# Optimization experiments

Measured on AMD Instinct MI355X. Metric: run time of the kernel, lower is better.

The kernel has to match this reference:

```python
import jax, jax.numpy as jnp
import numpy as np

N = 100000   # nodes
E = 1600000  # edges
F = 128      # in_feats
H = 4        # heads
D = 32       # out_feats per head
NEG_SLOPE = 0.2


def setup_inputs() -> dict:
    key = jax.random.key(0)
    k1, k2, k3, k4, k5, k6 = jax.random.split(key, 6)
    feat = jax.random.normal(k1, (N, F), dtype=jnp.float32)
    W = jax.random.normal(k2, (H * D, F), dtype=jnp.float32) * (1.0 / np.sqrt(F))
    attn_l = jax.random.normal(k3, (1, H, D), dtype=jnp.float32) * 0.1
    attn_r = jax.random.normal(k4, (1, H, D), dtype=jnp.float32) * 0.1
    src = jax.random.randint(k5, (E,), 0, N, dtype=jnp.int32)
    dst = jax.random.randint(k6, (E,), 0, N, dtype=jnp.int32)
    return {"feat": feat, "W": W, "attn_l": attn_l, "attn_r": attn_r, "src": src, "dst": dst}


def reference(feat, W, attn_l, attn_r, src, dst):
    # fc projection: [N, F] -> [N, H, D]
    h = (feat @ W.T).reshape(N, H, D)
    # per-node attention logits [N, H]
    el = jnp.sum(h * attn_l, axis=-1)
    er = jnp.sum(h * attn_r, axis=-1)
    # edge scores: el[src] + er[dst] -> leaky relu  [E, H]
    e = jax.nn.leaky_relu(el[src] + er[dst], negative_slope=NEG_SLOPE)
    # segment softmax over edges grouped by destination node, per head
    m = jax.ops.segment_max(e, dst, num_segments=N)          # [N, H]
    ex = jnp.exp(e - m[dst])                                 # [E, H]
    s = jax.ops.segment_sum(ex, dst, num_segments=N)         # [N, H]
    alpha = ex / s[dst]                                      # [E, H]
    # weighted sparse aggregation: out[dst] += alpha * h[src]
    msgs = alpha[:, :, None] * h[src]                        # [E, H, D]
    rst = jax.ops.segment_sum(msgs, dst, num_segments=N)     # [N, H, D]
    return rst
```

## Files before the change

### kernel.cpp

```cpp
#include <hip/hip_runtime.h>

constexpr int N_NODES = 100000;
constexpr int E_EDGES = 1600000;
constexpr int NBLK    = (N_NODES + 1023) / 1024;

typedef _Float16 f16;
typedef _Float16 f16x2 __attribute__((ext_vector_type(2)));
typedef _Float16 f16x4 __attribute__((ext_vector_type(4)));
typedef _Float16 f16x8 __attribute__((ext_vector_type(8)));
typedef float f32x4 __attribute__((ext_vector_type(4)));

__global__ __launch_bounds__(256) void k_gemm(const float* __restrict__ feat,
                                              const float* __restrict__ W,
                                              const float* __restrict__ attn_l,
                                              const float* __restrict__ attn_r,
                                              f16* __restrict__ h2,
                                              float* __restrict__ el,
                                              float* __restrict__ er) {
    __shared__ f16 Wlds[128 * 128];
    char* wb = (char*)Wlds;
    const int tid = threadIdx.x;

    {
        int n = tid >> 1;
        int kh = (tid & 1) * 64;
        const float* wsrc = W + n * 128 + kh;
#pragma unroll
        for (int q = 0; q < 8; ++q) {
            float4 u0 = *reinterpret_cast<const float4*>(wsrc + q * 8);
            float4 u1 = *reinterpret_cast<const float4*>(wsrc + q * 8 + 4);
            f16x8 v;
            v[0] = (f16)u0.x; v[1] = (f16)u0.y; v[2] = (f16)u0.z; v[3] = (f16)u0.w;
            v[4] = (f16)u1.x; v[5] = (f16)u1.y; v[6] = (f16)u1.z; v[7] = (f16)u1.w;
            unsigned byte = (unsigned)(n * 256 + kh * 2 + q * 16) ^ ((n & 7) << 4);
            *reinterpret_cast<f16x8*>(wb + byte) = v;
        }
    }
    __syncthreads();

    const int wav  = tid >> 6;
    const int lane = tid & 63;
    const int la = lane & 15;
    const int lb = lane >> 4;
    const int row0w = blockIdx.x * 64 + wav * 16;

    f16x8 ffrag[4];
    {
        int rowA = row0w + la;
        if (rowA >= N_NODES) rowA = N_NODES - 1;
        const float* ap = feat + (size_t)rowA * 128 + lb * 8;
#pragma unroll
        for (int kk = 0; kk < 4; ++kk) {
            float4 u0 = *reinterpret_cast<const float4*>(ap + kk * 32);
            float4 u1 = *reinterpret_cast<const float4*>(ap + kk * 32 + 4);
            f16x8 a;
            a[0] = (f16)u0.x; a[1] = (f16)u0.y; a[2] = (f16)u0.z; a[3] = (f16)u0.w;
            a[4] = (f16)u1.x; a[5] = (f16)u1.y; a[6] = (f16)u1.z; a[7] = (f16)u1.w;
            ffrag[kk] = a;
        }
    }

    f32x4 acc[8];
#pragma unroll
    for (int t = 0; t < 8; ++t) acc[t] = (f32x4){0.f, 0.f, 0.f, 0.f};

#pragma unroll
    for (int t = 0; t < 8; ++t) {
        int wrow = t * 16 + la;
#pragma unroll
        for (int kk = 0; kk < 4; ++kk) {
            unsigned byte = (unsigned)(wrow * 256 + (kk * 32 + lb * 8) * 2) ^ ((wrow & 7) << 4);
            f16x8 b = *reinterpret_cast<const f16x8*>(wb + byte);
            acc[t] = __builtin_amdgcn_mfma_f32_16x16x32_f16(b, ffrag[kk], acc[t], 0, 0, 0);
        }
    }

    const int row = row0w + la;
    const bool ok = row < N_NODES;
    if (ok) {
#pragma unroll
        for (int t = 0; t < 8; ++t) {
            f16x4 hv;
            hv.x = (f16)acc[t][0]; hv.y = (f16)acc[t][1];
            hv.z = (f16)acc[t][2]; hv.w = (f16)acc[t][3];
            *reinterpret_cast<f16x4*>(&h2[(size_t)row * 128 + t * 16 + lb * 4]) = hv;
        }
    }

    float sl[4] = {0.f, 0.f, 0.f, 0.f}, sr[4] = {0.f, 0.f, 0.f, 0.f};
#pragma unroll
    for (int t = 0; t < 8; ++t) {
        float4 alv = reinterpret_cast<const float4*>(attn_l)[t * 4 + lb];
        float4 arv = reinterpret_cast<const float4*>(attn_r)[t * 4 + lb];
        int g = t >> 1;
        sl[g] += acc[t][0] * alv.x + acc[t][1] * alv.y + acc[t][2] * alv.z + acc[t][3] * alv.w;
        sr[g] += acc[t][0] * arv.x + acc[t][1] * arv.y + acc[t][2] * arv.z + acc[t][3] * arv.w;
    }
#pragma unroll
    for (int g = 0; g < 4; ++g) {
        sl[g] += __shfl_xor(sl[g], 16, 64);
        sl[g] += __shfl_xor(sl[g], 32, 64);
        sr[g] += __shfl_xor(sr[g], 16, 64);
        sr[g] += __shfl_xor(sr[g], 32, 64);
    }
    if (lb == 0 && ok) {
        *reinterpret_cast<float4*>(el + (size_t)row * 4) = make_float4(sl[0], sl[1], sl[2], sl[3]);
        *reinterpret_cast<float4*>(er + (size_t)row * 4) = make_float4(sr[0], sr[1], sr[2], sr[3]);
    }
}

__global__ void k_hist(const int4* __restrict__ dst4, int* __restrict__ deg,
                       int4* __restrict__ rank4) {
    int t = blockIdx.x * blockDim.x + threadIdx.x;
    if (t < E_EDGES / 4) {
        int4 d = dst4[t];
        int r0 = atomicAdd(&deg[d.x], 1);
        int r1 = atomicAdd(&deg[d.y], 1);
        int r2 = atomicAdd(&deg[d.z], 1);
        int r3 = atomicAdd(&deg[d.w], 1);
        rank4[t] = make_int4(r0, r1, r2, r3);
    }
}

__global__ void k_bsum(const int* __restrict__ deg, int* __restrict__ aux) {
    int tid = threadIdx.x;
    int i0 = blockIdx.x * 1024 + tid * 4;
    int sum = 0;
#pragma unroll
    for (int j = 0; j < 4; ++j)
        if (i0 + j < N_NODES) sum += (deg[i0 + j] + 3) & ~3;
#pragma unroll
    for (int m = 32; m; m >>= 1) sum += __shfl_xor(sum, m, 64);
    __shared__ int wsums[4];
    if ((tid & 63) == 0) wsums[tid >> 6] = sum;
    __syncthreads();
    if (tid == 0) aux[blockIdx.x] = wsums[0] + wsums[1] + wsums[2] + wsums[3];
}

__global__ void k_scanaux(int* __restrict__ aux) {
    __shared__ int s[128];
    int i = threadIdx.x;
    int v = (i < NBLK) ? aux[i] : 0;
    s[i] = v;
    __syncthreads();
#pragma unroll
    for (int d = 1; d < 128; d <<= 1) {
        int t = (i >= d) ? s[i - d] : 0;
        __syncthreads();
        s[i] += t;
        __syncthreads();
    }
    if (i < NBLK) aux[i] = s[i] - v;
}

__global__ void k_bscan(const int* __restrict__ deg, const int* __restrict__ aux,
                        int* __restrict__ start, int* __restrict__ ssrc,
                        f16* __restrict__ h2, float* __restrict__ el) {
    if (blockIdx.x == 0 && threadIdx.x == 0) {
        float4 z = make_float4(0.f, 0.f, 0.f, 0.f);
        float4* hrow = reinterpret_cast<float4*>(h2 + (size_t)N_NODES * 128);
#pragma unroll
        for (int q = 0; q < 16; ++q) hrow[q] = z;
        *reinterpret_cast<float4*>(el + (size_t)N_NODES * 4) =
            make_float4(-1e4f, -1e4f, -1e4f, -1e4f);
    }
    int tid = threadIdx.x;
    int lane = tid & 63;
    int wid = tid >> 6;
    int i0 = blockIdx.x * 1024 + tid * 4;
    int v[4], pv[4];
#pragma unroll
    for (int j = 0; j < 4; ++j) {
        v[j]  = (i0 + j < N_NODES) ? deg[i0 + j] : 0;
        pv[j] = (v[j] + 3) & ~3;
    }
    int tsum = pv[0] + pv[1] + pv[2] + pv[3];
    int x = tsum;
#pragma unroll
    for (int d = 1; d < 64; d <<= 1) {
        int t = __shfl_up(x, d, 64);
        if (lane >= d) x += t;
    }
    __shared__ int wsums[4];
    if (lane == 63) wsums[wid] = x;
    __syncthreads();
    int base = aux[blockIdx.x];
#pragma unroll
    for (int w = 0; w < 4; ++w)
        if (w < wid) base += wsums[w];
    int p = base + x - tsum;
#pragma unroll
    for (int j = 0; j < 4; ++j) {
        if (i0 + j < N_NODES) {
            start[i0 + j] = p;
            for (int q = v[j]; q < pv[j]; ++q) ssrc[p + q] = N_NODES;
        }
        p += pv[j];
    }
}

__global__ void k_scatter(const int* __restrict__ src, const int* __restrict__ dst,
                          const int* __restrict__ rank, const int* __restrict__ start,
                          int* __restrict__ ssrc) {
    int e = blockIdx.x * blockDim.x + threadIdx.x;
    if (e < E_EDGES) ssrc[start[dst[e]] + rank[e]] = src[e];
}

__global__ __launch_bounds__(128) void k_aggr(const f16* __restrict__ h2,
                                              const float* __restrict__ el,
                                              const float* __restrict__ er,
                                              const int* __restrict__ ssrc,
                                              const int* __restrict__ start,
                                              const int* __restrict__ deg,
                                              float* __restrict__ out) {
    int n = blockIdx.x * 2 + (threadIdx.x >> 6);
    if (n >= N_NODES) return;
    int lane = threadIdx.x & 63;
    int g = lane >> 4;
    int d = deg[n];
    int pd = (d + 3) & ~3;
    int s0 = __builtin_amdgcn_readfirstlane(start[n]);
    float ern = er[n * 4 + g];

    f16x2 ac0 = {0, 0}, ac1 = {0, 0}, ac2 = {0, 0}, ac3 = {0, 0};
    f16x2 sw0 = {0, 0}, sw1 = {0, 0}, sw2 = {0, 0}, sw3 = {0, 0};

    for (int i = 0; i < pd; i += 4) {
        int n0 = ssrc[s0 + i];
        int n1 = ssrc[s0 + i + 1];
        int n2 = ssrc[s0 + i + 2];
        int n3 = ssrc[s0 + i + 3];
        float e0 = el[(size_t)n0 * 4 + g];
        float e1 = el[(size_t)n1 * 4 + g];
        float e2 = el[(size_t)n2 * 4 + g];
        float e3 = el[(size_t)n3 * 4 + g];
        f16x2 q0 = reinterpret_cast<const f16x2*>(h2 + (size_t)n0 * 128)[lane];
        f16x2 q1 = reinterpret_cast<const f16x2*>(h2 + (size_t)n1 * 128)[lane];
        f16x2 q2 = reinterpret_cast<const f16x2*>(h2 + (size_t)n2 * 128)[lane];
        f16x2 q3 = reinterpret_cast<const f16x2*>(h2 + (size_t)n3 * 128)[lane];

        float x0 = e0 + ern; x0 = fmaxf(x0, 0.2f * x0);
        float x1 = e1 + ern; x1 = fmaxf(x1, 0.2f * x1);
        float x2 = e2 + ern; x2 = fmaxf(x2, 0.2f * x2);
        float x3 = e3 + ern; x3 = fmaxf(x3, 0.2f * x3);
        float w0 = __expf(x0);
        float w1 = __expf(x1);
        float w2 = __expf(x2);
        float w3 = __expf(x3);

        f16 a0 = (f16)w0; f16x2 wv0 = {a0, a0};
        f16 a1 = (f16)w1; f16x2 wv1 = {a1, a1};
        f16 a2 = (f16)w2; f16x2 wv2 = {a2, a2};
        f16 a3 = (f16)w3; f16x2 wv3 = {a3, a3};

        ac0 += wv0 * q0; sw0 += wv0;
        ac1 += wv1 * q1; sw1 += wv1;
        ac2 += wv2 * q2; sw2 += wv2;
        ac3 += wv3 * q3; sw3 += wv3;
    }

    f16x2 ac = (ac0 + ac1) + (ac2 + ac3);
    f16x2 sw = (sw0 + sw1) + (sw2 + sw3);
    float swf = (float)sw[0];
    float inv = (d > 0) ? 1.0f / swf : 0.0f;
    float2 o = make_float2((float)ac[0] * inv, (float)ac[1] * inv);
    reinterpret_cast<float2*>(out + (size_t)n * 128)[lane] = o;
}

extern "C" void kernel_launch(void* const* d_in, const int* in_sizes, int n_in,
                              void* d_out, int out_size, void* d_ws, size_t ws_size,
                              hipStream_t stream) {
    const float* feat   = (const float*)d_in[0];
    const float* W      = (const float*)d_in[1];
    const float* attn_l = (const float*)d_in[2];
    const float* attn_r = (const float*)d_in[3];
    const int*   src    = (const int*)d_in[4];
    const int*   dst    = (const int*)d_in[5];
    float* out = (float*)d_out;

    f16*   h2    = (f16*)d_ws;
    float* el    = (float*)(h2 + (size_t)(N_NODES + 8) * 128);
    float* er    = el + (size_t)(N_NODES + 4) * 4;
    int*   deg   = (int*)(er + (size_t)N_NODES * 4);
    int*   start = deg + N_NODES;
    int*   rank  = start + N_NODES;
    int*   ssrc  = rank + E_EDGES;
    int*   aux   = ssrc + E_EDGES + 3 * N_NODES + 64;

    hipMemsetAsync(deg, 0, N_NODES * sizeof(int), stream);

    k_hist<<<(E_EDGES / 4 + 255) / 256, 256, 0, stream>>>((const int4*)dst, deg, (int4*)rank);
    k_gemm<<<(N_NODES + 63) / 64, 256, 0, stream>>>(feat, W, attn_l, attn_r, h2, el, er);
    k_bsum<<<NBLK, 256, 0, stream>>>(deg, aux);
    k_scanaux<<<1, 128, 0, stream>>>(aux);
    k_bscan<<<NBLK, 256, 0, stream>>>(deg, aux, start, ssrc, h2, el);
    k_scatter<<<(E_EDGES + 255) / 256, 256, 0, stream>>>(src, dst, rank, start, ssrc);
    k_aggr<<<(N_NODES + 1) / 2, 128, 0, stream>>>(h2, el, er, ssrc, start, deg, out);
}
```

Measured before the change: 211.7 us.

## Merge scan into single-block kernel and split aggregation wave into edge halves

Replaces the three-kernel degree scan (block sums, aux scan, block scan) with one 1024-thread single-block kernel where each thread scans 98 nodes serially, removing two launches and their dependencies. The aggregation kernel now has each half-wave process a different edge with 4 halfs per lane, then combines the halves with cross-lane shuffles. The softmax denominator is accumulated in fp32. The single-block scan has strided, uncoalesced per-thread reads and runs on one CU, and the aggregation adds shuffle-reduction overhead.

```diff
diff --git a/kernel.cpp b/kernel.cpp
--- a/kernel.cpp
+++ b/kernel.cpp
@@ -2,7 +2,6 @@
 
 constexpr int N_NODES = 100000;
 constexpr int E_EDGES = 1600000;
-constexpr int NBLK    = (N_NODES + 1023) / 1024;
 
 typedef _Float16 f16;
 typedef _Float16 f16x2 __attribute__((ext_vector_type(2)));
@@ -122,80 +121,48 @@
     }
 }
 
-__global__ void k_bsum(const int* __restrict__ deg, int* __restrict__ aux) {
-    int tid = threadIdx.x;
-    int i0 = blockIdx.x * 1024 + tid * 4;
+__global__ __launch_bounds__(1024) void k_scan(const int* __restrict__ deg,
+                                               int* __restrict__ start,
+                                               int* __restrict__ ssrc,
+                                               f16* __restrict__ h2,
+                                               float* __restrict__ el) {
+    const int t = threadIdx.x;
+    const int i0 = t * 98;
+    const int i1 = min(i0 + 98, N_NODES);
     int sum = 0;
-#pragma unroll
-    for (int j = 0; j < 4; ++j)
-        if (i0 + j < N_NODES) sum += (deg[i0 + j] + 3) & ~3;
-#pragma unroll
-    for (int m = 32; m; m >>= 1) sum += __shfl_xor(sum, m, 64);
-    __shared__ int wsums[4];
-    if ((tid & 63) == 0) wsums[tid >> 6] = sum;
+    for (int i = i0; i < i1; ++i) sum += (deg[i] + 3) & ~3;
+
+    int lane = t & 63, wid = t >> 6;
+    int x = sum;
+#pragma unroll
+    for (int d = 1; d < 64; d <<= 1) {
+        int v = __shfl_up(x, d, 64);
+        if (lane >= d) x += v;
+    }
+    __shared__ int wsum[16];
+    if (lane == 63) wsum[wid] = x;
     __syncthreads();
-    if (tid == 0) aux[blockIdx.x] = wsums[0] + wsums[1] + wsums[2] + wsums[3];
-}
-
-__global__ void k_scanaux(int* __restrict__ aux) {
-    __shared__ int s[128];
-    int i = threadIdx.x;
-    int v = (i < NBLK) ? aux[i] : 0;
-    s[i] = v;
-    __syncthreads();
-#pragma unroll
-    for (int d = 1; d < 128; d <<= 1) {
-        int t = (i >= d) ? s[i - d] : 0;
-        __syncthreads();
-        s[i] += t;
-        __syncthreads();
-    }
-    if (i < NBLK) aux[i] = s[i] - v;
-}
-
-__global__ void k_bscan(const int* __restrict__ deg, const int* __restrict__ aux,
-                        int* __restrict__ start, int* __restrict__ ssrc,
-                        f16* __restrict__ h2, float* __restrict__ el) {
-    if (blockIdx.x == 0 && threadIdx.x == 0) {
+    int base = 0;
+#pragma unroll
+    for (int w = 0; w < 16; ++w)
+        if (w < wid) base += wsum[w];
+
+    int p = base + x - sum;
+    for (int i = i0; i < i1; ++i) {
+        int v = deg[i];
+        int pv = (v + 3) & ~3;
+        start[i] = p;
+        for (int q = v; q < pv; ++q) ssrc[p + q] = N_NODES;
+        p += pv;
+    }
+
+    if (t == 0) {
         float4 z = make_float4(0.f, 0.f, 0.f, 0.f);
         float4* hrow = reinterpret_cast<float4*>(h2 + (size_t)N_NODES * 128);
 #pragma unroll
         for (int q = 0; q < 16; ++q) hrow[q] = z;
         *reinterpret_cast<float4*>(el + (size_t)N_NODES * 4) =
             make_float4(-1e4f, -1e4f, -1e4f, -1e4f);
-    }
-    int tid = threadIdx.x;
-    int lane = tid & 63;
-    int wid = tid >> 6;
-    int i0 = blockIdx.x * 1024 + tid * 4;
-    int v[4], pv[4];
-#pragma unroll
-    for (int j = 0; j < 4; ++j) {
-        v[j]  = (i0 + j < N_NODES) ? deg[i0 + j] : 0;
-        pv[j] = (v[j] + 3) & ~3;
-    }
-    int tsum = pv[0] + pv[1] + pv[2] + pv[3];
-    int x = tsum;
-#pragma unroll
-    for (int d = 1; d < 64; d <<= 1) {
-        int t = __shfl_up(x, d, 64);
-        if (lane >= d) x += t;
-    }
-    __shared__ int wsums[4];
-    if (lane == 63) wsums[wid] = x;
-    __syncthreads();
-    int base = aux[blockIdx.x];
-#pragma unroll
-    for (int w = 0; w < 4; ++w)
-        if (w < wid) base += wsums[w];
-    int p = base + x - tsum;
-#pragma unroll
-    for (int j = 0; j < 4; ++j) {
-        if (i0 + j < N_NODES) {
-            start[i0 + j] = p;
-            for (int q = v[j]; q < pv[j]; ++q) ssrc[p + q] = N_NODES;
-        }
-        p += pv[j];
     }
 }
 
@@ -216,55 +183,55 @@
     int n = blockIdx.x * 2 + (threadIdx.x >> 6);
     if (n >= N_NODES) return;
     int lane = threadIdx.x & 63;
-    int g = lane >> 4;
+    int half = lane >> 5;
+    int l5 = lane & 31;
+    int g = l5 >> 3;
     int d = deg[n];
     int pd = (d + 3) & ~3;
     int s0 = __builtin_amdgcn_readfirstlane(start[n]);
     float ern = er[n * 4 + g];
 
-    f16x2 ac0 = {0, 0}, ac1 = {0, 0}, ac2 = {0, 0}, ac3 = {0, 0};
-    f16x2 sw0 = {0, 0}, sw1 = {0, 0}, sw2 = {0, 0}, sw3 = {0, 0};
+    f16x4 acA = {0, 0, 0, 0}, acB = {0, 0, 0, 0};
+    float swA = 0.f, swB = 0.f;
 
     for (int i = 0; i < pd; i += 4) {
         int n0 = ssrc[s0 + i];
         int n1 = ssrc[s0 + i + 1];
         int n2 = ssrc[s0 + i + 2];
         int n3 = ssrc[s0 + i + 3];
-        float e0 = el[(size_t)n0 * 4 + g];
-        float e1 = el[(size_t)n1 * 4 + g];
-        float e2 = el[(size_t)n2 * 4 + g];
-        float e3 = el[(size_t)n3 * 4 + g];
-        f16x2 q0 = reinterpret_cast<const f16x2*>(h2 + (size_t)n0 * 128)[lane];
-        f16x2 q1 = reinterpret_cast<const f16x2*>(h2 + (size_t)n1 * 128)[lane];
-        f16x2 q2 = reinterpret_cast<const f16x2*>(h2 + (size_t)n2 * 128)[lane];
-        f16x2 q3 = reinterpret_cast<const f16x2*>(h2 + (size_t)n3 * 128)[lane];
-
-        float x0 = e0 + ern; x0 = fmaxf(x0, 0.2f * x0);
-        float x1 = e1 + ern; x1 = fmaxf(x1, 0.2f * x1);
-        float x2 = e2 + ern; x2 = fmaxf(x2, 0.2f * x2);
-        float x3 = e3 + ern; x3 = fmaxf(x3, 0.2f * x3);
-        float w0 = __expf(x0);
-        float w1 = __expf(x1);
-        float w2 = __expf(x2);
-        float w3 = __expf(x3);
-
-        f16 a0 = (f16)w0; f16x2 wv0 = {a0, a0};
-        f16 a1 = (f16)w1; f16x2 wv1 = {a1, a1};
-        f16 a2 = (f16)w2; f16x2 wv2 = {a2, a2};
-        f16 a3 = (f16)w3; f16x2 wv3 = {a3, a3};
-
-        ac0 += wv0 * q0; sw0 += wv0;
-        ac1 += wv1 * q1; sw1 += wv1;
-        ac2 += wv2 * q2; sw2 += wv2;
-        ac3 += wv3 * q3; sw3 += wv3;
-    }
-
-    f16x2 ac = (ac0 + ac1) + (ac2 + ac3);
-    f16x2 sw = (sw0 + sw1) + (sw2 + sw3);
-    float swf = (float)sw[0];
-    float inv = (d > 0) ? 1.0f / swf : 0.0f;
-    float2 o = make_float2((float)ac[0] * inv, (float)ac[1] * inv);
-    reinterpret_cast<float2*>(out + (size_t)n * 128)[lane] = o;
+        int nA = half ? n1 : n0;
+        int nB = half ? n3 : n2;
+        float eA = el[(size_t)nA * 4 + g];
+        float eB = el[(size_t)nB * 4 + g];
+        f16x4 qA = *reinterpret_cast<const f16x4*>(h2 + (size_t)nA * 128 + l5 * 4);
+        f16x4 qB = *reinterpret_cast<const f16x4*>(h2 + (size_t)nB * 128 + l5 * 4);
+
+        float xA = eA + ern; xA = fmaxf(xA, 0.2f * xA);
+        float xB = eB + ern; xB = fmaxf(xB, 0.2f * xB);
+        float wA = __expf(xA);
+        float wB = __expf(xB);
+
+        f16 hA = (f16)wA; f16x4 wvA = {hA, hA, hA, hA};
+        f16 hB = (f16)wB; f16x4 wvB = {hB, hB, hB, hB};
+        acA += wvA * qA; swA += wA;
+        acB += wvB * qB; swB += wB;
+    }
+
+    f16x4 ac = acA + acB;
+    float swv = swA + swB;
+    union { f16x4 v; int u[2]; } uu; uu.v = ac;
+    int o0 = __shfl_xor(uu.u[0], 32, 64);
+    int o1 = __shfl_xor(uu.u[1], 32, 64);
+    union { int u[2]; f16x4 v; } vv; vv.u[0] = o0; vv.u[1] = o1;
+    ac += vv.v;
+    swv += __shfl_xor(swv, 32, 64);
+
+    float inv = (d > 0) ? 1.0f / swv : 0.0f;
+    if (half == 0) {
+        float4 o = make_float4((float)ac[0] * inv, (float)ac[1] * inv,
+                               (float)ac[2] * inv, (float)ac[3] * inv);
+        *reinterpret_cast<float4*>(out + (size_t)n * 128 + l5 * 4) = o;
+    }
 }
 
 extern "C" void kernel_launch(void* const* d_in, const int* in_sizes, int n_in,
@@ -285,15 +252,12 @@
     int*   start = deg + N_NODES;
     int*   rank  = start + N_NODES;
     int*   ssrc  = rank + E_EDGES;
-    int*   aux   = ssrc + E_EDGES + 3 * N_NODES + 64;
 
     hipMemsetAsync(deg, 0, N_NODES * sizeof(int), stream);
 
     k_hist<<<(E_EDGES / 4 + 255) / 256, 256, 0, stream>>>((const int4*)dst, deg, (int4*)rank);
     k_gemm<<<(N_NODES + 63) / 64, 256, 0, stream>>>(feat, W, attn_l, attn_r, h2, el, er);
-    k_bsum<<<NBLK, 256, 0, stream>>>(deg, aux);
-    k_scanaux<<<1, 128, 0, stream>>>(aux);
-    k_bscan<<<NBLK, 256, 0, stream>>>(deg, aux, start, ssrc, h2, el);
+    k_scan<<<1, 1024, 0, stream>>>(deg, start, ssrc, h2, el);
     k_scatter<<<(E_EDGES + 255) / 256, 256, 0, stream>>>(src, dst, rank, start, ssrc);
     k_aggr<<<(N_NODES + 1) / 2, 128, 0, stream>>>(h2, el, er, ssrc, start, deg, out);
 }
```

After: 440.6 us. +108.1%, slower.
